# Kernel optimization log

Measured on AMD Instinct MI355X. Metric: run time of the kernel, lower is better.

## Reference

```python
import jax, jax.numpy as jnp
import numpy as np

TEMP = 0.05            # self.temp
NUM_INSTANCES = 16     # self.num_instances


def _l2norm(x):
    return x / jnp.linalg.norm(x, axis=-1, keepdims=True)


def setup_inputs() -> dict:
    key = jax.random.key(0)
    ks = jax.random.split(key, 6)
    B, D, N, K, NDATA = 256, 2048, 32768, 8192, 100000
    inputs = jax.random.normal(ks[0], (B, D), jnp.float32)
    # memory bank rows are kept unit-norm by the momentum update; init normalized
    features = _l2norm(jax.random.normal(ks[1], (N, D), jnp.float32))
    kmeans_centeroids = jax.random.normal(ks[2], (K, D), jnp.float32)
    targets = jax.random.randint(ks[3], (B,), 0, N)
    kmeans_pids = jax.random.randint(ks[4], (NDATA,), 0, K)
    indexes = jax.random.randint(ks[5], (B,), 0, NDATA)
    return {"inputs": inputs, "features": features,
            "kmeans_centeroids": kmeans_centeroids, "targets": targets,
            "kmeans_pids": kmeans_pids, "indexes": indexes, "neg_size": 20}


def reference(inputs, features, kmeans_centeroids, targets, kmeans_pids,
              indexes, neg_size):
    B = inputs.shape[0]
    K = kmeans_centeroids.shape[0]
    x = _l2norm(inputs)                                   # F.normalize(inputs, dim=1)
    outputs = x @ features.T                              # CM.forward: [B, N]
    finch_pos = jnp.take_along_axis(outputs, targets[:, None], axis=1)  # [B,1]
    kmeans_score = x @ kmeans_centeroids.T                # [B, K]
    batch_kmeans_pids = kmeans_pids[indexes]              # [B]
    # scatter_(-2) own kmeans cluster, then take top-neg_size negatives
    masked = jax.lax.stop_gradient(kmeans_score)          # detach().clone()
    masked = masked.at[jnp.arange(B), batch_kmeans_pids].set(-2.0)
    _, sel_ind_neg = jax.lax.top_k(masked, neg_size)      # [B, neg_size]
    kmeans_chosen_neg = jnp.take_along_axis(kmeans_score, sel_ind_neg, axis=1)
    mixed_score = jnp.concatenate([finch_pos, kmeans_chosen_neg], axis=1) / TEMP
    # confidence mask: per group of NUM_INSTANCES (first half of batch),
    # sample agrees with the group's modal kmeans pid (np.bincount().argmax())
    half = B // 2
    g = batch_kmeans_pids[:half].reshape(-1, NUM_INSTANCES)        # [G, I]
    counts = jax.nn.one_hot(g, K, dtype=jnp.int32).sum(axis=1)     # [G, K]
    mode = jnp.argmax(counts, axis=1)                              # ties -> smallest id
    mask_half = (g == mode[:, None]).reshape(-1).astype(jnp.float32)
    confidence_mask = jnp.concatenate([mask_half, mask_half])      # [B]
    # CE(mixed_score, 0) per-sample, confidence-weighted mean
    ce_neg = -jax.nn.log_softmax(mixed_score, axis=1)[:, 0]
    neg_con_loss = (confidence_mask * ce_neg).mean()
    # CE(outputs/temp, targets) mean
    logp = jax.nn.log_softmax(outputs / TEMP, axis=1)
    ce_main = -jnp.take_along_axis(logp, targets[:, None], axis=1).mean()
    return 0.2 * neg_con_loss + ce_main
```

## Files before the change

kernel.cpp:

```cpp
#include <hip/hip_runtime.h>
#include <stdint.h>

typedef __attribute__((ext_vector_type(8))) short short8;
typedef __attribute__((ext_vector_type(4))) float floatx4;

__device__ __forceinline__ unsigned short f2b(float f) {
    union { float f; uint32_t u; } v; v.f = f;
    uint32_t u = v.u;
    return (unsigned short)((u + 0x7FFFu + ((u >> 16) & 1u)) >> 16);
}

__device__ __forceinline__ uint32_t pk2(float a, float b) {
    union { float f; uint32_t u; } x, y; x.f = a; y.f = b;
    uint32_t ua = x.u + 0x8000u, ub = y.u + 0x8000u;
    return (ua >> 16) | (ub & 0xFFFF0000u);
}

__device__ __forceinline__ void async16(const void* g, void* l) {
    __builtin_amdgcn_global_load_lds(
        (const __attribute__((address_space(1))) void*)g,
        (__attribute__((address_space(3))) void*)l, 16, 0, 0);
}

__global__ void norm_kernel(const float* __restrict__ in,
                            unsigned short* __restrict__ xb, int D) {
    int b = blockIdx.x, t = threadIdx.x;
    const float* row = in + (size_t)b * D;
    float ss = 0.f;
    for (int i = t * 4; i < D; i += 1024) {
        float4 v = *(const float4*)(row + i);
        ss += v.x * v.x + v.y * v.y + v.z * v.z + v.w * v.w;
    }
    for (int off = 32; off > 0; off >>= 1) ss += __shfl_down(ss, off);
    __shared__ float wsum[4];
    __shared__ float rn_sh;
    if ((t & 63) == 0) wsum[t >> 6] = ss;
    __syncthreads();
    if (t == 0) rn_sh = rsqrtf(wsum[0] + wsum[1] + wsum[2] + wsum[3]);
    __syncthreads();
    float rn = rn_sh;
    unsigned short* orow = xb + (size_t)b * D;
    for (int i = t * 4; i < D; i += 1024) {
        float4 v = *(const float4*)(row + i);
        ushort4 o;
        o.x = f2b(v.x * rn); o.y = f2b(v.y * rn);
        o.z = f2b(v.z * rn); o.w = f2b(v.w * rn);
        *(ushort4*)(orow + i) = o;
    }
}

#define BKk 64
__global__ __launch_bounds__(256, 4)
void gemm_kernel(const unsigned short* __restrict__ xb,
                 const float* __restrict__ featB,
                 const float* __restrict__ centB,
                 const int* __restrict__ targets,
                 float* __restrict__ S, float* __restrict__ pos,
                 float* __restrict__ km,
                 int D, int K, int nbF) {
    __shared__ __align__(16) unsigned short Alds[256 * BKk];
    __shared__ __align__(16) unsigned short Blds[32 * BKk];

    const int t = threadIdx.x;
    const int w = t >> 6, l = t & 63;
    const bool isFeat = ((int)blockIdx.x < nbF);
    const int n0 = (isFeat ? (int)blockIdx.x : ((int)blockIdx.x - nbF)) * 32;
    const float* Bsrc = isFeat ? featB : centB;

    floatx4 acc[4][2];
#pragma unroll
    for (int ti = 0; ti < 4; ++ti)
#pragma unroll
        for (int tj = 0; tj < 2; ++tj)
            acc[ti][tj] = (floatx4){0.f, 0.f, 0.f, 0.f};

    const int kIters = D / BKk;
    const int brow = t >> 3, bq = t & 7;
    const float* bg0 = Bsrc + (size_t)(n0 + brow) * D + bq * 8;
    const int bslot = (bq ^ (brow & 7)) * 16;
    const char* xbB = (const char*)xb;

    for (int kt = 0; kt < kIters; ++kt) {
#pragma unroll
        for (int j = 0; j < 8; ++j) {
            int slin = j * 256 + t;
            int r = slin >> 3;
            int cg = (slin & 7) ^ (r & 7);
            async16(xbB + (size_t)r * (D * 2) + kt * (BKk * 2) + cg * 16,
                    (char*)Alds + slin * 16);
        }
        {
            const float* bg = bg0 + kt * BKk;
            float4 f0 = *(const float4*)(bg);
            float4 f1 = *(const float4*)(bg + 4);
            uint4 p;
            p.x = pk2(f0.x, f0.y); p.y = pk2(f0.z, f0.w);
            p.z = pk2(f1.x, f1.y); p.w = pk2(f1.z, f1.w);
            *(uint4*)((char*)Blds + brow * 128 + bslot) = p;
        }
        __syncthreads();

#pragma unroll
        for (int s = 0; s < 2; ++s) {
            short8 aF[4], bF[2];
#pragma unroll
            for (int ti = 0; ti < 4; ++ti) {
                int R = w * 64 + ti * 16 + (l & 15);
                int g = s * 4 + (l >> 4);
                aF[ti] = *(const short8*)((const char*)Alds +
                          R * 128 + ((g ^ (R & 7)) * 16));
            }
#pragma unroll
            for (int tj = 0; tj < 2; ++tj) {
                int Rn = tj * 16 + (l & 15);
                int g = s * 4 + (l >> 4);
                bF[tj] = *(const short8*)((const char*)Blds +
                          Rn * 128 + ((g ^ (Rn & 7)) * 16));
            }
#pragma unroll
            for (int ti = 0; ti < 4; ++ti)
#pragma unroll
                for (int tj = 0; tj < 2; ++tj)
                    acc[ti][tj] = __builtin_amdgcn_mfma_f32_16x16x32_bf16(
                        aF[ti], bF[tj], acc[ti][tj], 0, 0, 0);
        }
        __syncthreads();
    }

    if (isFeat) {
#pragma unroll
        for (int ti = 0; ti < 4; ++ti) {
#pragma unroll
            for (int r = 0; r < 4; ++r) {
                int row = w * 64 + ti * 16 + ((l >> 4) << 2) + r;
                int tr = targets[row];
                int col0 = n0 + (l & 15);
                float e = 0.f;
#pragma unroll
                for (int tj = 0; tj < 2; ++tj) {
                    float c = acc[ti][tj][r];
                    e += __expf(c * 20.0f);
                    if (tr == col0 + tj * 16) pos[row] = c;
                }
                e += __shfl_xor(e, 1); e += __shfl_xor(e, 2);
                e += __shfl_xor(e, 4); e += __shfl_xor(e, 8);
                if ((l & 15) == 0) atomicAdd(&S[row], e);
            }
        }
    } else {
#pragma unroll
        for (int ti = 0; ti < 4; ++ti) {
#pragma unroll
            for (int r = 0; r < 4; ++r) {
                int row = w * 64 + ti * 16 + ((l >> 4) << 2) + r;
                size_t base = (size_t)row * K + n0 + (l & 15);
#pragma unroll
                for (int tj = 0; tj < 2; ++tj)
                    km[base + tj * 16] = acc[ti][tj][r];
            }
        }
    }
}

__global__ __launch_bounds__(256, 4)
void topk_kernel(const float* __restrict__ kmr,
                 const int* __restrict__ pids,
                 const int* __restrict__ idxs,
                 const int* __restrict__ negsz,
                 float* __restrict__ topv, int K) {
    int b = blockIdx.x, t = threadIdx.x;
    int w = t >> 6, l = t & 63;
    const float* row = kmr + (size_t)b * K;
    float v[32];
#pragma unroll
    for (int k = 0; k < 32; ++k) v[k] = row[k * 256 + t];
    int gi = pids[idxs[b]];
    if ((gi & 255) == t) {
        int kk = gi >> 8;
#pragma unroll
        for (int k = 0; k < 32; ++k) if (k == kk) v[k] = -1e30f;
    }
    float bv = v[0]; int bk = 0;
#pragma unroll
    for (int k = 1; k < 32; ++k) if (v[k] > bv) { bv = v[k]; bk = k; }

    __shared__ float rv[4];
    __shared__ int rg[4];
    int ns = *negsz; if (ns > 32) ns = 32;
    for (int j = 0; j < ns; ++j) {
        float mv = bv; int mg = bk * 256 + t;
#pragma unroll
        for (int off = 1; off < 64; off <<= 1) {
            float ov = __shfl_xor(mv, off);
            int og = __shfl_xor(mg, off);
            if (ov > mv) { mv = ov; mg = og; }
        }
        if (l == 0) { rv[w] = mv; rg[w] = mg; }
        __syncthreads();
        float gv = rv[0]; int gg = rg[0];
#pragma unroll
        for (int ww = 1; ww < 4; ++ww)
            if (rv[ww] > gv) { gv = rv[ww]; gg = rg[ww]; }
        if (t == 0) topv[b * 32 + j] = gv;
        if ((gg & 255) == t) {
            int kk = gg >> 8;
#pragma unroll
            for (int k = 0; k < 32; ++k) if (k == kk) v[k] = -1e30f;
            bv = v[0]; bk = 0;
#pragma unroll
            for (int k = 1; k < 32; ++k) if (v[k] > bv) { bv = v[k]; bk = k; }
        }
        __syncthreads();
    }
}

__global__ void final_kernel(const float* __restrict__ S,
                             const float* __restrict__ pos,
                             const float* __restrict__ topv,
                             const int* __restrict__ pids,
                             const int* __restrict__ idxs,
                             const int* __restrict__ negsz,
                             float* __restrict__ out, int B) {
    __shared__ int pid_sh[256];
    __shared__ int mode_sh[16];
    __shared__ float red[256];
    int t = threadIdx.x;
    if (t < B) pid_sh[t] = pids[idxs[t]];
    __syncthreads();
    int half = B >> 1;
    int G = half / 16;
    if (t < G) {
        int bestPid = 0x7FFFFFFF, bestCnt = -1;
        for (int i = 0; i < 16; ++i) {
            int p = pid_sh[t * 16 + i];
            int c = 0;
            for (int j = 0; j < 16; ++j) c += (pid_sh[t * 16 + j] == p) ? 1 : 0;
            if (c > bestCnt || (c == bestCnt && p < bestPid)) { bestCnt = c; bestPid = p; }
        }
        mode_sh[t] = bestPid;
    }
    __syncthreads();
    float contrib = 0.f;
    if (t < B) {
        int hb = (t < half) ? t : t - half;
        float mask = (pid_sh[hb] == mode_sh[hb / 16]) ? 1.f : 0.f;
        int ns = *negsz; if (ns > 32) ns = 32;
        float p20 = pos[t] * 20.0f;
        float m = p20;
        for (int j = 0; j < ns; ++j) m = fmaxf(m, topv[t * 32 + j] * 20.0f);
        float se = __expf(p20 - m);
        for (int j = 0; j < ns; ++j) se += __expf(topv[t * 32 + j] * 20.0f - m);
        float ce_neg = m + logf(se) - p20;
        float ce_main = logf(S[t]) - p20;
        contrib = (0.2f * mask * ce_neg + ce_main) / (float)B;
    }
    red[t] = contrib;
    __syncthreads();
    for (int s = 128; s > 0; s >>= 1) {
        if (t < s) red[t] += red[t + s];
        __syncthreads();
    }
    if (t == 0) out[0] = red[0];
}

extern "C" void kernel_launch(void* const* d_in, const int* in_sizes, int n_in,
                              void* d_out, int out_size, void* d_ws, size_t ws_size,
                              hipStream_t stream) {
    const float* inputs   = (const float*)d_in[0];
    const float* features = (const float*)d_in[1];
    const float* cents    = (const float*)d_in[2];
    const int*   targets  = (const int*)d_in[3];
    const int*   pids     = (const int*)d_in[4];
    const int*   idxs     = (const int*)d_in[5];
    const int*   negsz    = (const int*)d_in[6];
    float* out = (float*)d_out;

    int Bb = in_sizes[3];
    int Dd = in_sizes[0] / Bb;
    int Nn = in_sizes[1] / Dd;
    int Kk = in_sizes[2] / Dd;

    char* ws = (char*)d_ws;
    unsigned short* xb = (unsigned short*)ws;
    size_t o = (size_t)Bb * Dd * 2;
    float* km   = (float*)(ws + o); o += (size_t)Bb * Kk * 4;
    float* S    = (float*)(ws + o); o += (size_t)Bb * 4;
    float* pos  = (float*)(ws + o); o += (size_t)Bb * 4;
    float* topv = (float*)(ws + o); o += (size_t)Bb * 32 * 4;

    hipMemsetAsync(S, 0, (size_t)Bb * 4, stream);
    norm_kernel<<<Bb, 256, 0, stream>>>(inputs, xb, Dd);
    int nbF = Nn / 32, nbC = Kk / 32;
    gemm_kernel<<<nbF + nbC, 256, 0, stream>>>(xb, features, cents, targets,
                                               S, pos, km, Dd, Kk, nbF);
    topk_kernel<<<Bb, 256, 0, stream>>>(km, pids, idxs, negsz, topv, Kk);
    final_kernel<<<1, 256, 0, stream>>>(S, pos, topv, pids, idxs, negsz, out, Bb);
}
```

Baseline: 526.6 us.

## Double-buffer GEMM A tile, load B directly to registers, widen N tile

Restructures the fused GEMM: each block now covers 64 columns instead of 32, using a 2x2 wave grid where each wave does 128 rows by 32 columns. The A tile in LDS is double-buffered with async loads issued one k-step ahead. The fp32 B operand is prefetched straight into registers and packed to bf16 without going through LDS. The aim is to overlap global loads with MFMA work and halve how often the A panel is re-read per output column, at the cost of more registers, more LDS, lower occupancy (launch bounds 2) and half as many blocks.

```diff
diff --git a/kernel.cpp b/kernel.cpp
--- a/kernel.cpp
+++ b/kernel.cpp
@@ -50,7 +50,7 @@
 }
 
 #define BKk 64
-__global__ __launch_bounds__(256, 4)
+__global__ __launch_bounds__(256, 2)
 void gemm_kernel(const unsigned short* __restrict__ xb,
                  const float* __restrict__ featB,
                  const float* __restrict__ centB,
@@ -58,83 +58,115 @@
                  float* __restrict__ S, float* __restrict__ pos,
                  float* __restrict__ km,
                  int D, int K, int nbF) {
-    __shared__ __align__(16) unsigned short Alds[256 * BKk];
-    __shared__ __align__(16) unsigned short Blds[32 * BKk];
+    __shared__ __align__(16) unsigned short Alds[2][256 * BKk];
 
     const int t = threadIdx.x;
     const int w = t >> 6, l = t & 63;
+    const int wr = w >> 1, wc = w & 1;
     const bool isFeat = ((int)blockIdx.x < nbF);
-    const int n0 = (isFeat ? (int)blockIdx.x : ((int)blockIdx.x - nbF)) * 32;
+    const int n0 = (isFeat ? (int)blockIdx.x : ((int)blockIdx.x - nbF)) * 64;
     const float* Bsrc = isFeat ? featB : centB;
 
-    floatx4 acc[4][2];
-#pragma unroll
-    for (int ti = 0; ti < 4; ++ti)
+    floatx4 acc[8][2];
+#pragma unroll
+    for (int ti = 0; ti < 8; ++ti)
 #pragma unroll
         for (int tj = 0; tj < 2; ++tj)
             acc[ti][tj] = (floatx4){0.f, 0.f, 0.f, 0.f};
 
     const int kIters = D / BKk;
-    const int brow = t >> 3, bq = t & 7;
-    const float* bg0 = Bsrc + (size_t)(n0 + brow) * D + bq * 8;
-    const int bslot = (bq ^ (brow & 7)) * 16;
     const char* xbB = (const char*)xb;
-
-    for (int kt = 0; kt < kIters; ++kt) {
+    const float* bgw = Bsrc + (size_t)(n0 + wc * 32 + (l & 15)) * D
+                            + ((l >> 4) * 8);
+
+    auto stageA = [&](int nb, int ktn) {
 #pragma unroll
         for (int j = 0; j < 8; ++j) {
             int slin = j * 256 + t;
             int r = slin >> 3;
             int cg = (slin & 7) ^ (r & 7);
-            async16(xbB + (size_t)r * (D * 2) + kt * (BKk * 2) + cg * 16,
-                    (char*)Alds + slin * 16);
-        }
-        {
-            const float* bg = bg0 + kt * BKk;
-            float4 f0 = *(const float4*)(bg);
-            float4 f1 = *(const float4*)(bg + 4);
-            uint4 p;
-            p.x = pk2(f0.x, f0.y); p.y = pk2(f0.z, f0.w);
-            p.z = pk2(f1.x, f1.y); p.w = pk2(f1.z, f1.w);
-            *(uint4*)((char*)Blds + brow * 128 + bslot) = p;
-        }
-        __syncthreads();
-
+            async16(xbB + (size_t)r * (D * 2) + (size_t)ktn * (BKk * 2) + cg * 16,
+                    (char*)(&Alds[nb][0]) + slin * 16);
+        }
+    };
+    auto loadB = [&](float4 (&F)[2][2][2], int ktn) {
+#pragma unroll
+        for (int tj = 0; tj < 2; ++tj)
+#pragma unroll
+            for (int s = 0; s < 2; ++s)
+#pragma unroll
+                for (int q = 0; q < 2; ++q)
+                    F[tj][s][q] = *(const float4*)(bgw + (size_t)tj * 16 * D
+                                                   + ktn * BKk + s * 32 + q * 4);
+    };
+    auto compute = [&](int cb, const float4 (&F)[2][2][2]) {
+        const char* Ab = (const char*)(&Alds[cb][0]);
 #pragma unroll
         for (int s = 0; s < 2; ++s) {
-            short8 aF[4], bF[2];
-#pragma unroll
-            for (int ti = 0; ti < 4; ++ti) {
-                int R = w * 64 + ti * 16 + (l & 15);
+            short8 aF[8], bF[2];
+#pragma unroll
+            for (int ti = 0; ti < 8; ++ti) {
+                int R = wr * 128 + ti * 16 + (l & 15);
                 int g = s * 4 + (l >> 4);
-                aF[ti] = *(const short8*)((const char*)Alds +
-                          R * 128 + ((g ^ (R & 7)) * 16));
+                aF[ti] = *(const short8*)(Ab + R * 128 + ((g ^ (R & 7)) * 16));
             }
 #pragma unroll
             for (int tj = 0; tj < 2; ++tj) {
-                int Rn = tj * 16 + (l & 15);
-                int g = s * 4 + (l >> 4);
-                bF[tj] = *(const short8*)((const char*)Blds +
-                          Rn * 128 + ((g ^ (Rn & 7)) * 16));
+                uint32_t u0 = pk2(F[tj][s][0].x, F[tj][s][0].y);
+                uint32_t u1 = pk2(F[tj][s][0].z, F[tj][s][0].w);
+                uint32_t u2 = pk2(F[tj][s][1].x, F[tj][s][1].y);
+                uint32_t u3 = pk2(F[tj][s][1].z, F[tj][s][1].w);
+                union { uint32_t u[4]; short8 v; } cvt;
+                cvt.u[0] = u0; cvt.u[1] = u1; cvt.u[2] = u2; cvt.u[3] = u3;
+                bF[tj] = cvt.v;
             }
 #pragma unroll
-            for (int ti = 0; ti < 4; ++ti)
+            for (int ti = 0; ti < 8; ++ti)
 #pragma unroll
                 for (int tj = 0; tj < 2; ++tj)
                     acc[ti][tj] = __builtin_amdgcn_mfma_f32_16x16x32_bf16(
                         aF[ti], bF[tj], acc[ti][tj], 0, 0, 0);
         }
-        __syncthreads();
+    };
+
+    float4 Bf[2][2][2], Bg[2][2][2];
+
+    stageA(0, 0);
+    loadB(Bf, 0);
+
+    for (int kt = 0; kt < kIters; kt += 2) {
+        {
+            int ktn = kt + 1 < kIters ? kt + 1 : kIters - 1;
+            stageA(1, ktn);
+            loadB(Bg, ktn);
+            asm volatile("s_waitcnt vmcnt(16)" ::: "memory");
+            __builtin_amdgcn_s_barrier();
+            asm volatile("" ::: "memory");
+            compute(0, Bf);
+            asm volatile("" ::: "memory");
+            __builtin_amdgcn_s_barrier();
+        }
+        {
+            int ktn = kt + 2 < kIters ? kt + 2 : kIters - 1;
+            stageA(0, ktn);
+            loadB(Bf, ktn);
+            asm volatile("s_waitcnt vmcnt(16)" ::: "memory");
+            __builtin_amdgcn_s_barrier();
+            asm volatile("" ::: "memory");
+            compute(1, Bg);
+            asm volatile("" ::: "memory");
+            __builtin_amdgcn_s_barrier();
+        }
     }
 
     if (isFeat) {
 #pragma unroll
-        for (int ti = 0; ti < 4; ++ti) {
+        for (int ti = 0; ti < 8; ++ti) {
 #pragma unroll
             for (int r = 0; r < 4; ++r) {
-                int row = w * 64 + ti * 16 + ((l >> 4) << 2) + r;
+                int row = wr * 128 + ti * 16 + ((l >> 4) << 2) + r;
                 int tr = targets[row];
-                int col0 = n0 + (l & 15);
+                int col0 = n0 + wc * 32 + (l & 15);
                 float e = 0.f;
 #pragma unroll
                 for (int tj = 0; tj < 2; ++tj) {
@@ -149,11 +181,11 @@
         }
     } else {
 #pragma unroll
-        for (int ti = 0; ti < 4; ++ti) {
+        for (int ti = 0; ti < 8; ++ti) {
 #pragma unroll
             for (int r = 0; r < 4; ++r) {
-                int row = w * 64 + ti * 16 + ((l >> 4) << 2) + r;
-                size_t base = (size_t)row * K + n0 + (l & 15);
+                int row = wr * 128 + ti * 16 + ((l >> 4) << 2) + r;
+                size_t base = (size_t)row * K + n0 + wc * 32 + (l & 15);
 #pragma unroll
                 for (int tj = 0; tj < 2; ++tj)
                     km[base + tj * 16] = acc[ti][tj][r];
@@ -290,7 +322,7 @@
 
     hipMemsetAsync(S, 0, (size_t)Bb * 4, stream);
     norm_kernel<<<Bb, 256, 0, stream>>>(inputs, xb, Dd);
-    int nbF = Nn / 32, nbC = Kk / 32;
+    int nbF = Nn / 64, nbC = Kk / 64;
     gemm_kernel<<<nbF + nbC, 256, 0, stream>>>(xb, features, cents, targets,
                                                S, pos, km, Dd, Kk, nbF);
     topk_kernel<<<Bb, 256, 0, stream>>>(km, pids, idxs, negsz, topv, Kk);
```

After: 600.1 us. 1.14x slower.
